# Optimization experiments

Measured on AMD Instinct MI355X. Metric: run time of the kernel, lower is better.

The kernel has to match this reference:

```python
import jax, jax.numpy as jnp
import numpy as np


def _swiglu(h):
    a, b = jnp.split(h, 2, axis=-1)
    return jax.nn.silu(a) * b


def setup_inputs() -> dict:
    key = jax.random.key(0)
    ks = jax.random.split(key, 12)
    B, T, D = 4, 2048, 1024
    HD = 4096          # dense FFN hidden (swiglu -> fc1 out 2*HD)
    S, K = 1024, 4     # ssm d_state, d_conv
    E, HE = 8, 512     # n_experts, expert hidden (swiglu)
    s = 0.02
    w = lambda k_, shape: jax.random.normal(k_, shape, jnp.float32) * s
    return dict(
        x=jax.random.normal(ks[0], (B, T, D), jnp.float32),
        rW=w(ks[1], (3, D)), rb=jnp.zeros((3,), jnp.float32),
        d1W=w(ks[2], (2 * HD, D)), d1b=jnp.zeros((2 * HD,), jnp.float32),
        d2W=w(ks[3], (D, HD)), d2b=jnp.zeros((D,), jnp.float32),
        sW_in=w(ks[4], (S, D)), sb_in=jnp.zeros((S,), jnp.float32),
        sW_conv=w(ks[5], (S, S, K)), sb_conv=jnp.zeros((S,), jnp.float32),
        sW_out=w(ks[6], (D, S)), sb_out=jnp.zeros((D,), jnp.float32),
        mW=w(ks[7], (E, D)), mb=jnp.zeros((E,), jnp.float32),
        eW1=w(ks[8], (E, 2 * HE, D)), eb1=jnp.zeros((E, 2 * HE), jnp.float32),
        eW2=w(ks[9], (E, D, HE)), eb2=jnp.zeros((E, D), jnp.float32),
        k=2,
    )


def reference(x, rW, rb, d1W, d1b, d2W, d2b,
              sW_in, sb_in, sW_conv, sb_conv, sW_out, sb_out,
              mW, mb, eW1, eb1, eW2, eb2, k):
    # ---- branch router (token-level softmax, temperature=1) ----
    bw = jax.nn.softmax(x @ rW.T + rb, axis=-1)              # [B,T,3]

    # ---- branch 0: dense swiglu FFN ----
    dense = _swiglu(x @ d1W.T + d1b) @ d2W.T + d2b           # [B,T,D]

    # ---- branch 1: SSM layer (causal conv, groups=1, gate=1) ----
    h = (x @ sW_in.T + sb_in).transpose(0, 2, 1)             # [B,S,T]
    Kc = sW_conv.shape[-1]
    conv = jax.lax.conv_general_dilated(
        h, sW_conv, window_strides=(1,), padding=[(Kc - 1, 0)],
        dimension_numbers=('NCH', 'OIH', 'NCH'))
    seq = (conv + sb_conv[None, :, None]).transpose(0, 2, 1)  # [B,T,S]
    ssm = seq @ sW_out.T + sb_out                             # [B,T,D]

    # ---- branch 2: MoE (top-k softmax router, dense-dispatch reference) ----
    E = mW.shape[0]
    logits = x @ mW.T + mb                                    # [B,T,E]
    vals, idx = jax.lax.top_k(logits, k)                      # [B,T,k]
    wk = jax.nn.softmax(vals, axis=-1)
    combine = jnp.sum(jax.nn.one_hot(idx, E, dtype=x.dtype) * wk[..., None], axis=-2)  # [B,T,E]
    h1 = _swiglu(jnp.einsum('btd,efd->btef', x, eW1) + eb1)   # [B,T,E,HE]
    eout = jnp.einsum('bteh,edh->bted', h1, eW2) + eb2        # [B,T,E,D]
    moe = jnp.einsum('bted,bte->btd', eout, combine)          # [B,T,D]

    return bw[..., 0:1] * dense + bw[..., 1:2] * ssm + bw[..., 2:3] * moe
```

## Files before the change

kernel.cpp:

```cpp
#include <hip/hip_runtime.h>
#include <hip/hip_bf16.h>
#include <cstdint>

typedef __bf16 bf16_t;
typedef __bf16 bf16x8 __attribute__((ext_vector_type(8)));
typedef float f32x4 __attribute__((ext_vector_type(4)));

#define DEV_INLINE __device__ __forceinline__

#define NTOK 8192
#define DDIM 1024
#define HDIM 4096
#define SDIM 1024
#define NEXP 8
#define HEXP 512
#define TSEQ 2048
#define MAXTILES 136
#define MAXROWS (MAXTILES * 128)

#define VMCNT(n) asm volatile("s_waitcnt vmcnt(" #n ")" ::: "memory")
#define BARF() asm volatile("s_barrier" ::: "memory")

__global__ __launch_bounds__(256) void k_f32_to_bf16(const float* __restrict__ src,
                                                     bf16_t* __restrict__ dst, int n8) {
  int i = blockIdx.x * 256 + threadIdx.x;
  if (i >= n8) return;
  const float4* s = (const float4*)src + (size_t)i * 2;
  float4 v0 = s[0], v1 = s[1];
  bf16x8 o;
  o[0] = (bf16_t)v0.x; o[1] = (bf16_t)v0.y; o[2] = (bf16_t)v0.z; o[3] = (bf16_t)v0.w;
  o[4] = (bf16_t)v1.x; o[5] = (bf16_t)v1.y; o[6] = (bf16_t)v1.z; o[7] = (bf16_t)v1.w;
  *((bf16x8*)dst + i) = o;
}

__global__ __launch_bounds__(256) void k_convw(const float* __restrict__ src,
                                               bf16_t* __restrict__ dst) {
  int i = blockIdx.x * 256 + threadIdx.x;
  size_t flat = (size_t)i * 8;
  int s = (int)(flat >> 12);
  int col = (int)(flat & 4095);
  int k = col >> 10;
  int si0 = col & 1023;
  const float* sp = src + (size_t)s * 4096 + k;
  bf16x8 o;
#pragma unroll
  for (int j = 0; j < 8; ++j) o[j] = (bf16_t)sp[(size_t)(si0 + j) * 4];
  *(bf16x8*)(dst + flat) = o;
}

__global__ __launch_bounds__(256) void k_zero(int* cnt, int* fill, int* idx,
                                              bf16_t* zpad) {
  int i = blockIdx.x * 256 + threadIdx.x;
  if (i < NEXP) { cnt[i] = 0; fill[i] = 0; }
  if (i < 128) zpad[i] = (bf16_t)0.f;
  if (i < MAXROWS) idx[i] = 0;
}

__global__ __launch_bounds__(1024) void k_count(const int* __restrict__ top2e,
                                                int* __restrict__ cnt) {
  __shared__ int hist[NEXP];
  const int tid = threadIdx.x;
  if (tid < NEXP) hist[tid] = 0;
  __syncthreads();
  int c[NEXP];
#pragma unroll
  for (int e = 0; e < NEXP; ++e) c[e] = 0;
#pragma unroll
  for (int j = 0; j < 2 * NTOK / 1024; ++j) {
    int v = top2e[j * 1024 + tid];
#pragma unroll
    for (int e = 0; e < NEXP; ++e) c[e] += (v == e) ? 1 : 0;
  }
#pragma unroll
  for (int e = 0; e < NEXP; ++e)
    for (int off = 32; off; off >>= 1) c[e] += __shfl_xor(c[e], off);
  if ((tid & 63) == 0) {
#pragma unroll
    for (int e = 0; e < NEXP; ++e) atomicAdd(&hist[e], c[e]);
  }
  __syncthreads();
  if (tid < NEXP) cnt[tid] = hist[tid];
}

__global__ void k_scan(const int* __restrict__ cnt, int* __restrict__ base,
                       int* __restrict__ ntiles, int* __restrict__ tile_e,
                       int* __restrict__ tile_row) {
  if (threadIdx.x == 0 && blockIdx.x == 0) {
    int b = 0, tt = 0;
    for (int e = 0; e < NEXP; ++e) {
      base[e] = b;
      int nt = (cnt[e] + 127) >> 7;
      for (int j = 0; j < nt; ++j) { tile_e[tt] = e; tile_row[tt] = b + j * 128; ++tt; }
      b += nt * 128;
    }
    *ntiles = tt;
  }
}

__global__ __launch_bounds__(256) void k_scatter(const int* __restrict__ top2e,
                                                 const float* __restrict__ top2w,
                                                 const int* __restrict__ base,
                                                 int* __restrict__ fill,
                                                 int* __restrict__ idx,
                                                 int* __restrict__ slotmap) {
  __shared__ int lcnt[NEXP];
  __shared__ int lbase[NEXP];
  const int tid = threadIdx.x;
  const int t = blockIdx.x * 256 + tid;
  if (tid < NEXP) lcnt[tid] = 0;
  __syncthreads();
  const int e0 = top2e[t * 2 + 0], e1 = top2e[t * 2 + 1];
  const int s0 = atomicAdd(&lcnt[e0], 1);
  const int s1 = atomicAdd(&lcnt[e1], 1);
  __syncthreads();
  if (tid < NEXP) lbase[tid] = atomicAdd(&fill[tid], lcnt[tid]);
  __syncthreads();
  const int p0 = base[e0] + lbase[e0] + s0;
  const int p1 = base[e1] + lbase[e1] + s1;
  idx[p0] = t; idx[p1] = t;
  slotmap[t * 2 + 0] = p0;
  slotmap[t * 2 + 1] = p1;
}

__global__ __launch_bounds__(256) void k_router(const float* __restrict__ x,
                                                const float* __restrict__ rW,
                                                const float* __restrict__ rb,
                                                const float* __restrict__ mW,
                                                const float* __restrict__ mb,
                                                float* __restrict__ bw3,
                                                int* __restrict__ top2e,
                                                float* __restrict__ top2w) {
  int wave = threadIdx.x >> 6, lane = threadIdx.x & 63;
  int t = blockIdx.x * 4 + wave;
  const float* xr = x + (size_t)t * DDIM;
  float xv[16];
#pragma unroll
  for (int i = 0; i < 16; i += 4) *(float4*)&xv[i] = *(const float4*)&xr[lane * 16 + i];
  float acc[11];
#pragma unroll
  for (int j = 0; j < 11; ++j) {
    const float* w = (j < 3) ? (rW + j * DDIM) : (mW + (j - 3) * DDIM);
    float s = 0.f;
#pragma unroll
    for (int i = 0; i < 16; i += 4) {
      float4 wv = *(const float4*)&w[lane * 16 + i];
      s += xv[i] * wv.x + xv[i + 1] * wv.y + xv[i + 2] * wv.z + xv[i + 3] * wv.w;
    }
    acc[j] = s;
  }
#pragma unroll
  for (int j = 0; j < 11; ++j)
    for (int off = 32; off; off >>= 1) acc[j] += __shfl_xor(acc[j], off);
  if (lane == 0) {
    float l0 = acc[0] + rb[0], l1 = acc[1] + rb[1], l2 = acc[2] + rb[2];
    float mx = fmaxf(l0, fmaxf(l1, l2));
    float e0 = expf(l0 - mx), e1 = expf(l1 - mx), e2 = expf(l2 - mx);
    float inv = 1.f / (e0 + e1 + e2);
    float w2 = e2 * inv;
    bw3[t * 3 + 0] = e0 * inv; bw3[t * 3 + 1] = e1 * inv; bw3[t * 3 + 2] = w2;
    float lg[8];
#pragma unroll
    for (int e = 0; e < 8; ++e) lg[e] = acc[3 + e] + mb[e];
    int i0 = 0;
#pragma unroll
    for (int e = 1; e < 8; ++e) if (lg[e] > lg[i0]) i0 = e;
    int i1 = -1;
#pragma unroll
    for (int e = 0; e < 8; ++e) {
      if (e == i0) continue;
      if (i1 < 0 || lg[e] > lg[i1]) i1 = e;
    }
    float ee = expf(lg[i1] - lg[i0]);
    float w0 = 1.f / (1.f + ee), w1 = ee / (1.f + ee);
    top2e[t * 2 + 0] = i0; top2e[t * 2 + 1] = i1;
    top2w[t * 2 + 0] = w2 * w0; top2w[t * 2 + 1] = w2 * w1;
  }
}

__global__ __launch_bounds__(256) void k_combine(const bf16_t* __restrict__ eo,
                                                 const int* __restrict__ slotmap,
                                                 const float* __restrict__ top2w,
                                                 float* __restrict__ out) {
  int wave = threadIdx.x >> 6, lane = threadIdx.x & 63;
  int t = blockIdx.x * 4 + wave;
  const int s0 = slotmap[t * 2 + 0], s1 = slotmap[t * 2 + 1];
  const float g0 = top2w[t * 2 + 0], g1 = top2w[t * 2 + 1];
  const bf16x8* r0 = (const bf16x8*)(eo + (size_t)s0 * DDIM);
  const bf16x8* r1 = (const bf16x8*)(eo + (size_t)s1 * DDIM);
  float* orow = out + (size_t)t * DDIM;
#pragma unroll
  for (int i = 0; i < 2; ++i) {
    const int d = lane + i * 64;
    bf16x8 a = r0[d], b = r1[d];
    float vo[8];
    *(float4*)&vo[0] = *(const float4*)&orow[d * 8];
    *(float4*)&vo[4] = *(const float4*)&orow[d * 8 + 4];
#pragma unroll
    for (int j = 0; j < 8; ++j) vo[j] += g0 * (float)a[j] + g1 * (float)b[j];
    *(float4*)&orow[d * 8] = *(float4*)&vo[0];
    *(float4*)&orow[d * 8 + 4] = *(float4*)&vo[4];
  }
}

DEV_INLINE void gload16(const bf16_t* g, bf16_t* l) {
  __builtin_amdgcn_global_load_lds((const __attribute__((address_space(1))) void*)g,
                                   (__attribute__((address_space(3))) void*)l, 16, 0, 0);
}

DEV_INLINE void blockmap(int K, int& bx, int& by) {
  const int nbx = gridDim.x, nby = gridDim.y;
  int id = blockIdx.x + nbx * blockIdx.y;
  const int nwg = nbx * nby;
  if ((nwg & 7) == 0) id = (id & 7) * (nwg >> 3) + (id >> 3);
  if ((nbx & 3) == 0 && (nby & 7) == 0 && K <= 2048) {
    const int nsx = nbx >> 2;
    const int sx = id & 3, r = id >> 2;
    const int sy = r & 7, st = r >> 3;
    bx = (st % nsx) * 4 + sx;
    by = (st / nsx) * 8 + sy;
  } else {
    bx = id % nbx;
    by = id / nbx;
  }
}

constexpr int EPI_BF16 = 0;
constexpr int EPI_OUT_W = 1;
constexpr int EPI_OUT_A = 2;
constexpr int EPI_SWIG = 4;

template <int EPI>
__global__ __launch_bounds__(256) void k_gemm(
    const bf16_t* __restrict__ A, const bf16_t* __restrict__ B,
    bf16_t* __restrict__ Cb, float* __restrict__ Cf,
    const float* __restrict__ bias, const float* __restrict__ scale, int sstride,
    const bf16_t* __restrict__ aux, int ldaux,
    int N, int K) {
  constexpr int BUF = 16384;
  __shared__ __align__(16) char lds[2 * BUF];

  const int tid = threadIdx.x;
  const int lane = tid & 63;
  const int wave = tid >> 6;
  const int lr = lane & 15;
  const int hi = lane >> 4;

  int bx, by;
  blockmap(K, bx, by);

  const int bm = by * 128;
  const int bn = bx * 128;
  const int wm = (wave >> 1) * 64;
  const int wn = (wave & 1) * 64;

  const int srow = tid >> 2;
  const int scol = 8 * ((tid & 3) ^ ((tid >> 3) & 3));
  const bf16_t* Asrc = A + (size_t)(bm + srow) * K + scol;
  const bf16_t* Bsrc = B + (size_t)(bn + srow) * K + scol;
  const size_t r64K = (size_t)64 * K;
  const int NT = K >> 5;

  f32x4 acc[4][4];
#pragma unroll
  for (int a = 0; a < 4; ++a)
#pragma unroll
    for (int b = 0; b < 4; ++b)
#pragma unroll
      for (int j = 0; j < 4; ++j) acc[a][b][j] = 0.f;

  auto stage = [&](int t) {
    char* l = lds + (t & 1) * BUF + tid * 16;
    const bf16_t* ga = Asrc + (size_t)t * 32;
    const bf16_t* gb = Bsrc + (size_t)t * 32;
    gload16(ga, (bf16_t*)l);
    gload16(ga + r64K, (bf16_t*)(l + 4096));
    gload16(gb, (bf16_t*)(l + 8192));
    gload16(gb + r64K, (bf16_t*)(l + 12288));
  };
  auto rdA = [&](int buf, int row) -> bf16x8 {
    int off = buf + (row << 6) + ((hi ^ ((row >> 1) & 3)) << 4);
    return *(const bf16x8*)(lds + off);
  };
  auto rdB = [&](int buf, int row) -> bf16x8 {
    int off = buf + 8192 + (row << 6) + ((hi ^ ((row >> 1) & 3)) << 4);
    return *(const bf16x8*)(lds + off);
  };

  stage(0);

  for (int t = 0; t < NT; ++t) {
    VMCNT(0);
    BARF();
    const int buf = (t & 1) * BUF;
    bf16x8 bfr[4], afr[4];
#pragma unroll
    for (int ni = 0; ni < 4; ++ni) bfr[ni] = rdB(buf, wn + ni * 16 + lr);
#pragma unroll
    for (int i = 0; i < 4; ++i) afr[i] = rdA(buf, wm + i * 16 + lr);
    if (t + 1 < NT) stage(t + 1);
    __builtin_amdgcn_s_setprio(1);
#pragma unroll
    for (int i = 0; i < 4; ++i)
#pragma unroll
      for (int ni = 0; ni < 4; ++ni)
        acc[i][ni] = __builtin_amdgcn_mfma_f32_16x16x32_bf16(afr[i], bfr[ni], acc[i][ni], 0, 0, 0);
    __builtin_amdgcn_s_setprio(0);
  }

  float bv[4];
#pragma unroll
  for (int ni = 0; ni < 4; ++ni) bv[ni] = bias[bn + wn + ni * 16 + lr];
#pragma unroll
  for (int mi = 0; mi < 4; ++mi) {
#pragma unroll
    for (int j = 0; j < 4; ++j) {
      const int rowg = bm + wm + mi * 16 + hi * 4 + j;
      float sc = 0.f;
      if constexpr (EPI == EPI_OUT_W || EPI == EPI_OUT_A)
        sc = scale[(size_t)rowg * sstride];
#pragma unroll
      for (int ni = 0; ni < 4; ++ni) {
        const int colg = bn + wn + ni * 16 + lr;
        float v = acc[mi][ni][j] + bv[ni];
        if constexpr (EPI == EPI_BF16) {
          Cb[(size_t)rowg * N + colg] = (bf16_t)v;
        } else if constexpr (EPI == EPI_OUT_W) {
          Cf[(size_t)rowg * N + colg] = sc * v;
        } else if constexpr (EPI == EPI_OUT_A) {
          Cf[(size_t)rowg * N + colg] += sc * v;
        } else {
          float bb = (float)aux[(size_t)rowg * ldaux + colg];
          float s = v / (1.f + __expf(-v));
          Cb[(size_t)rowg * N + colg] = (bf16_t)(s * bb);
        }
      }
    }
  }
}

__global__ __launch_bounds__(256) void k_gemm_conv(
    const bf16_t* __restrict__ h, const bf16_t* __restrict__ Bw,
    bf16_t* __restrict__ Cb, const float* __restrict__ bias,
    const bf16_t* __restrict__ zpad) {
  constexpr int N = SDIM;
  constexpr int K = SDIM * 4;
  constexpr int BUF = 16384;
  __shared__ __align__(16) char lds[2 * BUF];

  const int tid = threadIdx.x;
  const int lane = tid & 63;
  const int wave = tid >> 6;
  const int lr = lane & 15;
  const int hi = lane >> 4;

  int bx, by;
  blockmap(K, bx, by);

  const int bm = by * 128;
  const int bn = bx * 128;
  const int wm = (wave >> 1) * 64;
  const int wn = (wave & 1) * 64;

  const int srow = tid >> 2;
  const int scol = 8 * ((tid & 3) ^ ((tid >> 3) & 3));
  const int row0 = bm + srow;
  const int tt0 = row0 & (TSEQ - 1);
  const bf16_t* Bsrc = Bw + (size_t)(bn + srow) * K + scol;
  const size_t r64K = (size_t)64 * K;
  const int NT = K >> 5;

  f32x4 acc[4][4];
#pragma unroll
  for (int a = 0; a < 4; ++a)
#pragma unroll
    for (int b = 0; b < 4; ++b)
#pragma unroll
      for (int j = 0; j < 4; ++j) acc[a][b][j] = 0.f;

  auto stage = [&](int t) {
    char* l = lds + (t & 1) * BUF + tid * 16;
    const int k = t >> 5;
    const int si = (t & 31) * 32 + scol;
    const bf16_t* ga0 = (tt0 + k >= 3)
        ? h + (size_t)(row0 + k - 3) * SDIM + si : zpad;
    const bf16_t* ga1 = h + (size_t)(row0 + 64 + k - 3) * SDIM + si;
    gload16(ga0, (bf16_t*)l);
    gload16(ga1, (bf16_t*)(l + 4096));
    const bf16_t* gb = Bsrc + (size_t)t * 32;
    gload16(gb, (bf16_t*)(l + 8192));
    gload16(gb + r64K, (bf16_t*)(l + 12288));
  };
  auto rdA = [&](int buf, int row) -> bf16x8 {
    int off = buf + (row << 6) + ((hi ^ ((row >> 1) & 3)) << 4);
    return *(const bf16x8*)(lds + off);
  };
  auto rdB = [&](int buf, int row) -> bf16x8 {
    int off = buf + 8192 + (row << 6) + ((hi ^ ((row >> 1) & 3)) << 4);
    return *(const bf16x8*)(lds + off);
  };

  stage(0);

  for (int t = 0; t < NT; ++t) {
    VMCNT(0);
    BARF();
    const int buf = (t & 1) * BUF;
    bf16x8 bfr[4], afr[4];
#pragma unroll
    for (int ni = 0; ni < 4; ++ni) bfr[ni] = rdB(buf, wn + ni * 16 + lr);
#pragma unroll
    for (int i = 0; i < 4; ++i) afr[i] = rdA(buf, wm + i * 16 + lr);
    if (t + 1 < NT) stage(t + 1);
    __builtin_amdgcn_s_setprio(1);
#pragma unroll
    for (int i = 0; i < 4; ++i)
#pragma unroll
      for (int ni = 0; ni < 4; ++ni)
        acc[i][ni] = __builtin_amdgcn_mfma_f32_16x16x32_bf16(afr[i], bfr[ni], acc[i][ni], 0, 0, 0);
    __builtin_amdgcn_s_setprio(0);
  }

  float bv[4];
#pragma unroll
  for (int ni = 0; ni < 4; ++ni) bv[ni] = bias[bn + wn + ni * 16 + lr];
#pragma unroll
  for (int mi = 0; mi < 4; ++mi) {
#pragma unroll
    for (int j = 0; j < 4; ++j) {
      const int rowg = bm + wm + mi * 16 + hi * 4 + j;
#pragma unroll
      for (int ni = 0; ni < 4; ++ni) {
        const int colg = bn + wn + ni * 16 + lr;
        Cb[(size_t)rowg * N + colg] = (bf16_t)(acc[mi][ni][j] + bv[ni]);
      }
    }
  }
}

template <int EPI, bool GA>
__global__ __launch_bounds__(256) void k_moe_gemm(
    const bf16_t* __restrict__ A, const bf16_t* __restrict__ Bw, size_t zB, int boff,
    bf16_t* __restrict__ Cb,
    const float* __restrict__ bias, int bstride,
    const bf16_t* __restrict__ aux,
    const int* __restrict__ ntiles_p, const int* __restrict__ tile_e,
    const int* __restrict__ tile_row, const int* __restrict__ idx,
    int N, int K) {
  constexpr int BUF = 16384;
  __shared__ __align__(16) char lds[2 * BUF];

  const int tid = threadIdx.x;
  const int lane = tid & 63;
  const int wave = tid >> 6;
  const int lr = lane & 15;
  const int hi = lane >> 4;

  const int nbx = gridDim.x, nby = gridDim.y;
  int id = blockIdx.x + nbx * blockIdx.y;
  const int nwg = nbx * nby;
  if ((nwg & 7) == 0) id = (id & 7) * (nwg >> 3) + (id >> 3);
  const int bx = id % nbx;
  const int by = id / nbx;

  const int ntiles = *ntiles_p;
  if (bx >= ntiles) return;
  const int e = tile_e[bx];
  const int bm = tile_row[bx];
  const int bn = by * 128;
  const int wm = (wave >> 1) * 64;
  const int wn = (wave & 1) * 64;

  const int srow = tid >> 2;
  const int scol = 8 * ((tid & 3) ^ ((tid >> 3) & 3));
  const int atok0 = GA ? idx[bm + srow] : (bm + srow);
  const int atok1 = GA ? idx[bm + srow + 64] : (bm + srow + 64);
  const bf16_t* Asrc0 = A + (size_t)atok0 * K + scol;
  const bf16_t* Asrc1 = A + (size_t)atok1 * K + scol;
  const bf16_t* Bsrc = Bw + (size_t)e * zB + (size_t)(boff + bn + srow) * K + scol;
  const size_t r64K = (size_t)64 * K;
  const int NT = K >> 5;

  f32x4 acc[4][4];
#pragma unroll
  for (int a = 0; a < 4; ++a)
#pragma unroll
    for (int b = 0; b < 4; ++b)
#pragma unroll
      for (int j = 0; j < 4; ++j) acc[a][b][j] = 0.f;

  auto stage = [&](int t) {
    char* l = lds + (t & 1) * BUF + tid * 16;
    gload16(Asrc0 + (size_t)t * 32, (bf16_t*)l);
    gload16(Asrc1 + (size_t)t * 32, (bf16_t*)(l + 4096));
    gload16(Bsrc + (size_t)t * 32, (bf16_t*)(l + 8192));
    gload16(Bsrc + (size_t)t * 32 + r64K, (bf16_t*)(l + 12288));
  };
  auto rdA = [&](int buf, int row) -> bf16x8 {
    int off = buf + (row << 6) + ((hi ^ ((row >> 1) & 3)) << 4);
    return *(const bf16x8*)(lds + off);
  };
  auto rdB = [&](int buf, int row) -> bf16x8 {
    int off = buf + 8192 + (row << 6) + ((hi ^ ((row >> 1) & 3)) << 4);
    return *(const bf16x8*)(lds + off);
  };

  stage(0);

  for (int t = 0; t < NT; ++t) {
    VMCNT(0);
    BARF();
    const int buf = (t & 1) * BUF;
    bf16x8 bfr[4], afr[4];
#pragma unroll
    for (int ni = 0; ni < 4; ++ni) bfr[ni] = rdB(buf, wn + ni * 16 + lr);
#pragma unroll
    for (int i = 0; i < 4; ++i) afr[i] = rdA(buf, wm + i * 16 + lr);
    if (t + 1 < NT) stage(t + 1);
    __builtin_amdgcn_s_setprio(1);
#pragma unroll
    for (int i = 0; i < 4; ++i)
#pragma unroll
      for (int ni = 0; ni < 4; ++ni)
        acc[i][ni] = __builtin_amdgcn_mfma_f32_16x16x32_bf16(afr[i], bfr[ni], acc[i][ni], 0, 0, 0);
    __builtin_amdgcn_s_setprio(0);
  }

  const float* bp = bias + (size_t)e * bstride + boff;
  float bv[4];
#pragma unroll
  for (int ni = 0; ni < 4; ++ni) bv[ni] = bp[bn + wn + ni * 16 + lr];
#pragma unroll
  for (int mi = 0; mi < 4; ++mi) {
#pragma unroll
    for (int j = 0; j < 4; ++j) {
      const int slot = bm + wm + mi * 16 + hi * 4 + j;
#pragma unroll
      for (int ni = 0; ni < 4; ++ni) {
        const int colg = bn + wn + ni * 16 + lr;
        float v = acc[mi][ni][j] + bv[ni];
        if constexpr (EPI == EPI_BF16) {
          Cb[(size_t)slot * N + colg] = (bf16_t)v;
        } else {
          float bb = (float)aux[(size_t)slot * N + colg];
          float s = v / (1.f + __expf(-v));
          Cb[(size_t)slot * N + colg] = (bf16_t)(s * bb);
        }
      }
    }
  }
}

extern "C" void kernel_launch(void* const* d_in, const int* in_sizes, int n_in,
                              void* d_out, int out_size, void* d_ws, size_t ws_size,
                              hipStream_t stream) {
  (void)in_sizes; (void)n_in; (void)out_size; (void)ws_size;
  const float* x    = (const float*)d_in[0];
  const float* rW   = (const float*)d_in[1];
  const float* rb   = (const float*)d_in[2];
  const float* d1W  = (const float*)d_in[3];
  const float* d1b  = (const float*)d_in[4];
  const float* d2W  = (const float*)d_in[5];
  const float* d2b  = (const float*)d_in[6];
  const float* sWin = (const float*)d_in[7];
  const float* sbin = (const float*)d_in[8];
  const float* sWc  = (const float*)d_in[9];
  const float* sbc  = (const float*)d_in[10];
  const float* sWo  = (const float*)d_in[11];
  const float* sbo  = (const float*)d_in[12];
  const float* mW   = (const float*)d_in[13];
  const float* mb   = (const float*)d_in[14];
  const float* eW1  = (const float*)d_in[15];
  const float* eb1  = (const float*)d_in[16];
  const float* eW2  = (const float*)d_in[17];
  const float* eb2  = (const float*)d_in[18];
  float* out = (float*)d_out;

  char* ws = (char*)d_ws;
  size_t off = 0;
  auto alloc = [&](size_t bytes) -> void* {
    void* p = ws + off;
    off += (bytes + 255) & ~(size_t)255;
    return p;
  };
  bf16_t* xb    = (bf16_t*)alloc((size_t)NTOK * DDIM * 2);
  bf16_t* wd1   = (bf16_t*)alloc((size_t)2 * HDIM * DDIM * 2);
  bf16_t* wd2   = (bf16_t*)alloc((size_t)DDIM * HDIM * 2);
  bf16_t* wsin  = (bf16_t*)alloc((size_t)SDIM * DDIM * 2);
  bf16_t* wconv = (bf16_t*)alloc((size_t)SDIM * SDIM * 4 * 2);
  bf16_t* wsout = (bf16_t*)alloc((size_t)DDIM * SDIM * 2);
  bf16_t* we1   = (bf16_t*)alloc((size_t)NEXP * 2 * HEXP * DDIM * 2);
  bf16_t* we2   = (bf16_t*)alloc((size_t)NEXP * DDIM * HEXP * 2);
  bf16_t* Cc    = (bf16_t*)alloc((size_t)NTOK * HDIM * 2);
  bf16_t* Dd    = (bf16_t*)alloc((size_t)NTOK * HDIM * 2);
  bf16_t* th    = (bf16_t*)alloc((size_t)NTOK * SDIM * 2);
  bf16_t* tsq   = (bf16_t*)alloc((size_t)NTOK * SDIM * 2);
  float*  bw3   = (float*)alloc((size_t)NTOK * 3 * 4);
  int*    top2e = (int*)alloc((size_t)NTOK * 2 * 4);
  float*  top2w = (float*)alloc((size_t)NTOK * 2 * 4);
  int*    slotm = (int*)alloc((size_t)NTOK * 2 * 4);
  int*    cnt   = (int*)alloc(NEXP * 4);
  int*    fill  = (int*)alloc(NEXP * 4);
  int*    basep = (int*)alloc((NEXP + 1) * 4);
  int*    ntl   = (int*)alloc(4);
  int*    t_e   = (int*)alloc(MAXTILES * 4);
  int*    t_row = (int*)alloc(MAXTILES * 4);
  int*    idx   = (int*)alloc(MAXROWS * 4);
  bf16_t* zpad  = (bf16_t*)alloc(256);
  bf16_t* eo    = Dd;

  k_f32_to_bf16<<<4096, 256, 0, stream>>>(x, xb, NTOK * DDIM / 8);
  k_f32_to_bf16<<<4096, 256, 0, stream>>>(d1W, wd1, 2 * HDIM * DDIM / 8);
  k_f32_to_bf16<<<2048, 256, 0, stream>>>(d2W, wd2, DDIM * HDIM / 8);
  k_f32_to_bf16<<<512, 256, 0, stream>>>(sWin, wsin, SDIM * DDIM / 8);
  k_convw<<<2048, 256, 0, stream>>>(sWc, wconv);
  k_f32_to_bf16<<<512, 256, 0, stream>>>(sWo, wsout, DDIM * SDIM / 8);
  k_f32_to_bf16<<<4096, 256, 0, stream>>>(eW1, we1, NEXP * 2 * HEXP * DDIM / 8);
  k_f32_to_bf16<<<2048, 256, 0, stream>>>(eW2, we2, NEXP * DDIM * HEXP / 8);
  k_zero<<<(MAXROWS + 255) / 256, 256, 0, stream>>>(cnt, fill, idx, zpad);
  k_router<<<2048, 256, 0, stream>>>(x, rW, rb, mW, mb, bw3, top2e, top2w);
  k_count<<<1, 1024, 0, stream>>>(top2e, cnt);
  k_scan<<<1, 64, 0, stream>>>(cnt, basep, ntl, t_e, t_row);
  k_scatter<<<NTOK / 256, 256, 0, stream>>>(top2e, top2w, basep, fill, idx, slotm);

  k_gemm<EPI_BF16><<<dim3(32, 64), 256, 0, stream>>>(
      xb, wd1 + (size_t)HDIM * DDIM, Dd, nullptr, d1b + HDIM, nullptr, 0, nullptr, 0,
      HDIM, DDIM);
  k_gemm<EPI_SWIG><<<dim3(32, 64), 256, 0, stream>>>(
      xb, wd1, Cc, nullptr, d1b, nullptr, 0, Dd, HDIM, HDIM, DDIM);
  k_gemm<EPI_OUT_W><<<dim3(8, 64), 256, 0, stream>>>(
      Cc, wd2, nullptr, out, d2b, bw3, 3, nullptr, 0, DDIM, HDIM);

  k_moe_gemm<EPI_BF16, true><<<dim3(MAXTILES, 4), 256, 0, stream>>>(
      xb, we1, (size_t)2 * HEXP * DDIM, HEXP, Dd, eb1, 2 * HEXP, nullptr,
      ntl, t_e, t_row, idx, HEXP, DDIM);
  k_moe_gemm<EPI_SWIG, true><<<dim3(MAXTILES, 4), 256, 0, stream>>>(
      xb, we1, (size_t)2 * HEXP * DDIM, 0, Cc, eb1, 2 * HEXP, Dd,
      ntl, t_e, t_row, idx, HEXP, DDIM);
  k_moe_gemm<EPI_BF16, false><<<dim3(MAXTILES, 8), 256, 0, stream>>>(
      Cc, we2, (size_t)DDIM * HEXP, 0, eo, eb2, DDIM, nullptr,
      ntl, t_e, t_row, idx, DDIM, HEXP);
  k_combine<<<NTOK / 4, 256, 0, stream>>>(eo, slotm, top2w, out);

  k_gemm<EPI_BF16><<<dim3(8, 64), 256, 0, stream>>>(
      xb, wsin, th, nullptr, sbin, nullptr, 0, nullptr, 0, SDIM, DDIM);
  k_gemm_conv<<<dim3(8, 64), 256, 0, stream>>>(th, wconv, tsq, sbc, zpad);
  k_gemm<EPI_OUT_A><<<dim3(8, 64), 256, 0, stream>>>(
      tsq, wsout, nullptr, out, sbo, bw3 + 1, 3, nullptr, 0, DDIM, SDIM);
}
```

Before: 669.9 us.

## Fuse SwiGLU gate and up GEMMs into one dual-accumulator kernel

The dense FC1 and the MoE expert FC1 each used to run as two GEMMs: one wrote the up half to a bf16 buffer, and the second read it back in a SwiGLU epilogue. They are now single kernels that stage A once, load both weight halves into a larger LDS buffer, keep two accumulator sets, and apply silu(a)*b directly in the epilogue. This removes a full intermediate write/read and one read of the activations. The cost is double the accumulator registers, which can lower occupancy or cause spills. The grouped block-swizzle mapping in blockmap is also dropped in favour of a plain row-major mapping, which may change L2 reuse.

After: 691.9 us. 3.3% more time.

```diff
diff --git a/kernel.cpp b/kernel.cpp
--- a/kernel.cpp
+++ b/kernel.cpp
@@ -207,34 +207,24 @@
                                    (__attribute__((address_space(3))) void*)l, 16, 0, 0);
 }
 
-DEV_INLINE void blockmap(int K, int& bx, int& by) {
+DEV_INLINE void blockmap(int& bx, int& by) {
   const int nbx = gridDim.x, nby = gridDim.y;
   int id = blockIdx.x + nbx * blockIdx.y;
   const int nwg = nbx * nby;
   if ((nwg & 7) == 0) id = (id & 7) * (nwg >> 3) + (id >> 3);
-  if ((nbx & 3) == 0 && (nby & 7) == 0 && K <= 2048) {
-    const int nsx = nbx >> 2;
-    const int sx = id & 3, r = id >> 2;
-    const int sy = r & 7, st = r >> 3;
-    bx = (st % nsx) * 4 + sx;
-    by = (st / nsx) * 8 + sy;
-  } else {
-    bx = id % nbx;
-    by = id / nbx;
-  }
+  bx = id % nbx;
+  by = id / nbx;
 }
 
 constexpr int EPI_BF16 = 0;
 constexpr int EPI_OUT_W = 1;
 constexpr int EPI_OUT_A = 2;
-constexpr int EPI_SWIG = 4;
 
 template <int EPI>
 __global__ __launch_bounds__(256) void k_gemm(
     const bf16_t* __restrict__ A, const bf16_t* __restrict__ B,
     bf16_t* __restrict__ Cb, float* __restrict__ Cf,
     const float* __restrict__ bias, const float* __restrict__ scale, int sstride,
-    const bf16_t* __restrict__ aux, int ldaux,
     int N, int K) {
   constexpr int BUF = 16384;
   __shared__ __align__(16) char lds[2 * BUF];
@@ -246,7 +236,7 @@
   const int hi = lane >> 4;
 
   int bx, by;
-  blockmap(K, bx, by);
+  blockmap(bx, by);
 
   const int bm = by * 128;
   const int bn = bx * 128;
@@ -326,13 +316,112 @@
           Cb[(size_t)rowg * N + colg] = (bf16_t)v;
         } else if constexpr (EPI == EPI_OUT_W) {
           Cf[(size_t)rowg * N + colg] = sc * v;
-        } else if constexpr (EPI == EPI_OUT_A) {
+        } else {
           Cf[(size_t)rowg * N + colg] += sc * v;
-        } else {
-          float bb = (float)aux[(size_t)rowg * ldaux + colg];
-          float s = v / (1.f + __expf(-v));
-          Cb[(size_t)rowg * N + colg] = (bf16_t)(s * bb);
         }
+      }
+    }
+  }
+}
+
+__global__ __launch_bounds__(256) void k_gemm_fc1(
+    const bf16_t* __restrict__ A, const bf16_t* __restrict__ Ba,
+    const bf16_t* __restrict__ Bb, bf16_t* __restrict__ C,
+    const float* __restrict__ bias_a, const float* __restrict__ bias_b,
+    int N, int K) {
+  constexpr int BUF = 24576;
+  __shared__ __align__(16) char lds[2 * BUF];
+
+  const int tid = threadIdx.x;
+  const int lane = tid & 63;
+  const int wave = tid >> 6;
+  const int lr = lane & 15;
+  const int hi = lane >> 4;
+
+  int bx, by;
+  blockmap(bx, by);
+
+  const int bm = by * 128;
+  const int bn = bx * 128;
+  const int wm = (wave >> 1) * 64;
+  const int wn = (wave & 1) * 64;
+
+  const int srow = tid >> 2;
+  const int scol = 8 * ((tid & 3) ^ ((tid >> 3) & 3));
+  const bf16_t* Asrc = A + (size_t)(bm + srow) * K + scol;
+  const bf16_t* Basrc = Ba + (size_t)(bn + srow) * K + scol;
+  const bf16_t* Bbsrc = Bb + (size_t)(bn + srow) * K + scol;
+  const size_t r64K = (size_t)64 * K;
+  const int NT = K >> 5;
+
+  f32x4 aca[4][4], acb[4][4];
+#pragma unroll
+  for (int a = 0; a < 4; ++a)
+#pragma unroll
+    for (int b = 0; b < 4; ++b)
+#pragma unroll
+      for (int j = 0; j < 4; ++j) { aca[a][b][j] = 0.f; acb[a][b][j] = 0.f; }
+
+  auto stage = [&](int t) {
+    char* l = lds + (t & 1) * BUF + tid * 16;
+    const bf16_t* ga = Asrc + (size_t)t * 32;
+    const bf16_t* gba = Basrc + (size_t)t * 32;
+    const bf16_t* gbb = Bbsrc + (size_t)t * 32;
+    gload16(ga, (bf16_t*)l);
+    gload16(ga + r64K, (bf16_t*)(l + 4096));
+    gload16(gba, (bf16_t*)(l + 8192));
+    gload16(gba + r64K, (bf16_t*)(l + 12288));
+    gload16(gbb, (bf16_t*)(l + 16384));
+    gload16(gbb + r64K, (bf16_t*)(l + 20480));
+  };
+  auto rd = [&](int base, int row) -> bf16x8 {
+    int off = base + (row << 6) + ((hi ^ ((row >> 1) & 3)) << 4);
+    return *(const bf16x8*)(lds + off);
+  };
+
+  stage(0);
+
+  for (int t = 0; t < NT; ++t) {
+    VMCNT(0);
+    BARF();
+    const int buf = (t & 1) * BUF;
+    bf16x8 afr[4], bfa[4], bfb[4];
+#pragma unroll
+    for (int i = 0; i < 4; ++i) afr[i] = rd(buf, wm + i * 16 + lr);
+#pragma unroll
+    for (int ni = 0; ni < 4; ++ni) bfa[ni] = rd(buf + 8192, wn + ni * 16 + lr);
+#pragma unroll
+    for (int ni = 0; ni < 4; ++ni) bfb[ni] = rd(buf + 16384, wn + ni * 16 + lr);
+    if (t + 1 < NT) stage(t + 1);
+    __builtin_amdgcn_s_setprio(1);
+#pragma unroll
+    for (int i = 0; i < 4; ++i)
+#pragma unroll
+      for (int ni = 0; ni < 4; ++ni) {
+        aca[i][ni] = __builtin_amdgcn_mfma_f32_16x16x32_bf16(afr[i], bfa[ni], aca[i][ni], 0, 0, 0);
+        acb[i][ni] = __builtin_amdgcn_mfma_f32_16x16x32_bf16(afr[i], bfb[ni], acb[i][ni], 0, 0, 0);
+      }
+    __builtin_amdgcn_s_setprio(0);
+  }
+
+  float bva[4], bvb[4];
+#pragma unroll
+  for (int ni = 0; ni < 4; ++ni) {
+    bva[ni] = bias_a[bn + wn + ni * 16 + lr];
+    bvb[ni] = bias_b[bn + wn + ni * 16 + lr];
+  }
+#pragma unroll
+  for (int mi = 0; mi < 4; ++mi) {
+#pragma unroll
+    for (int j = 0; j < 4; ++j) {
+      const int rowg = bm + wm + mi * 16 + hi * 4 + j;
+#pragma unroll
+      for (int ni = 0; ni < 4; ++ni) {
+        const int colg = bn + wn + ni * 16 + lr;
+        float va = aca[mi][ni][j] + bva[ni];
+        float vb = acb[mi][ni][j] + bvb[ni];
+        float s = va / (1.f + __expf(-va));
+        C[(size_t)rowg * N + colg] = (bf16_t)(s * vb);
       }
     }
   }
@@ -354,7 +443,7 @@
   const int hi = lane >> 4;
 
   int bx, by;
-  blockmap(K, bx, by);
+  blockmap(bx, by);
 
   const int bm = by * 128;
   const int bn = bx * 128;
@@ -437,16 +526,13 @@
   }
 }
 
-template <int EPI, bool GA>
-__global__ __launch_bounds__(256) void k_moe_gemm(
-    const bf16_t* __restrict__ A, const bf16_t* __restrict__ Bw, size_t zB, int boff,
-    bf16_t* __restrict__ Cb,
-    const float* __restrict__ bias, int bstride,
-    const bf16_t* __restrict__ aux,
+__global__ __launch_bounds__(256) void k_moe_fc1(
+    const bf16_t* __restrict__ A, const bf16_t* __restrict__ Bw, size_t zB,
+    bf16_t* __restrict__ C, const float* __restrict__ bias, int bstride,
     const int* __restrict__ ntiles_p, const int* __restrict__ tile_e,
     const int* __restrict__ tile_row, const int* __restrict__ idx,
     int N, int K) {
-  constexpr int BUF = 16384;
+  constexpr int BUF = 24576;
   __shared__ __align__(16) char lds[2 * BUF];
 
   const int tid = threadIdx.x;
@@ -472,26 +558,136 @@
 
   const int srow = tid >> 2;
   const int scol = 8 * ((tid & 3) ^ ((tid >> 3) & 3));
-  const int atok0 = GA ? idx[bm + srow] : (bm + srow);
-  const int atok1 = GA ? idx[bm + srow + 64] : (bm + srow + 64);
+  const int atok0 = idx[bm + srow];
+  const int atok1 = idx[bm + srow + 64];
   const bf16_t* Asrc0 = A + (size_t)atok0 * K + scol;
   const bf16_t* Asrc1 = A + (size_t)atok1 * K + scol;
-  const bf16_t* Bsrc = Bw + (size_t)e * zB + (size_t)(boff + bn + srow) * K + scol;
+  const bf16_t* Basrc = Bw + (size_t)e * zB + (size_t)(bn + srow) * K + scol;
+  const bf16_t* Bbsrc = Basrc + (size_t)HEXP * K;
   const size_t r64K = (size_t)64 * K;
   const int NT = K >> 5;
 
-  f32x4 acc[4][4];
+  f32x4 aca[4][4], acb[4][4];
 #pragma unroll
   for (int a = 0; a < 4; ++a)
 #pragma unroll
     for (int b = 0; b < 4; ++b)
 #pragma unroll
-      for (int j = 0; j < 4; ++j) acc[a][b][j] = 0.f;
+      for (int j = 0; j < 4; ++j) { aca[a][b][j] = 0.f; acb[a][b][j] = 0.f; }
 
   auto stage = [&](int t) {
     char* l = lds + (t & 1) * BUF + tid * 16;
     gload16(Asrc0 + (size_t)t * 32, (bf16_t*)l);
     gload16(Asrc1 + (size_t)t * 32, (bf16_t*)(l + 4096));
+    gload16(Basrc + (size_t)t * 32, (bf16_t*)(l + 8192));
+    gload16(Basrc + (size_t)t * 32 + r64K, (bf16_t*)(l + 12288));
+    gload16(Bbsrc + (size_t)t * 32, (bf16_t*)(l + 16384));
+    gload16(Bbsrc + (size_t)t * 32 + r64K, (bf16_t*)(l + 20480));
+  };
+  auto rd = [&](int base, int row) -> bf16x8 {
+    int off = base + (row << 6) + ((hi ^ ((row >> 1) & 3)) << 4);
+    return *(const bf16x8*)(lds + off);
+  };
+
+  stage(0);
+
+  for (int t = 0; t < NT; ++t) {
+    VMCNT(0);
+    BARF();
+    const int buf = (t & 1) * BUF;
+    bf16x8 afr[4], bfa[4], bfb[4];
+#pragma unroll
+    for (int i = 0; i < 4; ++i) afr[i] = rd(buf, wm + i * 16 + lr);
+#pragma unroll
+    for (int ni = 0; ni < 4; ++ni) bfa[ni] = rd(buf + 8192, wn + ni * 16 + lr);
+#pragma unroll
+    for (int ni = 0; ni < 4; ++ni) bfb[ni] = rd(buf + 16384, wn + ni * 16 + lr);
+    if (t + 1 < NT) stage(t + 1);
+    __builtin_amdgcn_s_setprio(1);
+#pragma unroll
+    for (int i = 0; i < 4; ++i)
+#pragma unroll
+      for (int ni = 0; ni < 4; ++ni) {
+        aca[i][ni] = __builtin_amdgcn_mfma_f32_16x16x32_bf16(afr[i], bfa[ni], aca[i][ni], 0, 0, 0);
+        acb[i][ni] = __builtin_amdgcn_mfma_f32_16x16x32_bf16(afr[i], bfb[ni], acb[i][ni], 0, 0, 0);
+      }
+    __builtin_amdgcn_s_setprio(0);
+  }
+
+  const float* bpa = bias + (size_t)e * bstride;
+  const float* bpb = bpa + HEXP;
+  float bva[4], bvb[4];
+#pragma unroll
+  for (int ni = 0; ni < 4; ++ni) {
+    bva[ni] = bpa[bn + wn + ni * 16 + lr];
+    bvb[ni] = bpb[bn + wn + ni * 16 + lr];
+  }
+#pragma unroll
+  for (int mi = 0; mi < 4; ++mi) {
+#pragma unroll
+    for (int j = 0; j < 4; ++j) {
+      const int slot = bm + wm + mi * 16 + hi * 4 + j;
+#pragma unroll
+      for (int ni = 0; ni < 4; ++ni) {
+        const int colg = bn + wn + ni * 16 + lr;
+        float va = aca[mi][ni][j] + bva[ni];
+        float vb = acb[mi][ni][j] + bvb[ni];
+        float s = va / (1.f + __expf(-va));
+        C[(size_t)slot * N + colg] = (bf16_t)(s * vb);
+      }
+    }
+  }
+}
+
+__global__ __launch_bounds__(256) void k_moe_fc2(
+    const bf16_t* __restrict__ A, const bf16_t* __restrict__ Bw, size_t zB,
+    bf16_t* __restrict__ Cb, const float* __restrict__ bias, int bstride,
+    const int* __restrict__ ntiles_p, const int* __restrict__ tile_e,
+    const int* __restrict__ tile_row,
+    int N, int K) {
+  constexpr int BUF = 16384;
+  __shared__ __align__(16) char lds[2 * BUF];
+
+  const int tid = threadIdx.x;
+  const int lane = tid & 63;
+  const int wave = tid >> 6;
+  const int lr = lane & 15;
+  const int hi = lane >> 4;
+
+  const int nbx = gridDim.x, nby = gridDim.y;
+  int id = blockIdx.x + nbx * blockIdx.y;
+  const int nwg = nbx * nby;
+  if ((nwg & 7) == 0) id = (id & 7) * (nwg >> 3) + (id >> 3);
+  const int bx = id % nbx;
+  const int by = id / nbx;
+
+  const int ntiles = *ntiles_p;
+  if (bx >= ntiles) return;
+  const int e = tile_e[bx];
+  const int bm = tile_row[bx];
+  const int bn = by * 128;
+  const int wm = (wave >> 1) * 64;
+  const int wn = (wave & 1) * 64;
+
+  const int srow = tid >> 2;
+  const int scol = 8 * ((tid & 3) ^ ((tid >> 3) & 3));
+  const bf16_t* Asrc = A + (size_t)(bm + srow) * K + scol;
+  const bf16_t* Bsrc = Bw + (size_t)e * zB + (size_t)(bn + srow) * K + scol;
+  const size_t r64K = (size_t)64 * K;
+  const int NT = K >> 5;
+
+  f32x4 acc[4][4];
+#pragma unroll
+  for (int a = 0; a < 4; ++a)
+#pragma unroll
+    for (int b = 0; b < 4; ++b)
+#pragma unroll
+      for (int j = 0; j < 4; ++j) acc[a][b][j] = 0.f;
+
+  auto stage = [&](int t) {
+    char* l = lds + (t & 1) * BUF + tid * 16;
+    gload16(Asrc + (size_t)t * 32, (bf16_t*)l);
+    gload16(Asrc + (size_t)t * 32 + r64K, (bf16_t*)(l + 4096));
     gload16(Bsrc + (size_t)t * 32, (bf16_t*)(l + 8192));
     gload16(Bsrc + (size_t)t * 32 + r64K, (bf16_t*)(l + 12288));
   };
@@ -525,7 +721,7 @@
     __builtin_amdgcn_s_setprio(0);
   }
 
-  const float* bp = bias + (size_t)e * bstride + boff;
+  const float* bp = bias + (size_t)e * bstride;
   float bv[4];
 #pragma unroll
   for (int ni = 0; ni < 4; ++ni) bv[ni] = bp[bn + wn + ni * 16 + lr];
@@ -537,14 +733,7 @@
 #pragma unroll
       for (int ni = 0; ni < 4; ++ni) {
         const int colg = bn + wn + ni * 16 + lr;
-        float v = acc[mi][ni][j] + bv[ni];
-        if constexpr (EPI == EPI_BF16) {
-          Cb[(size_t)slot * N + colg] = (bf16_t)v;
-        } else {
-          float bb = (float)aux[(size_t)slot * N + colg];
-          float s = v / (1.f + __expf(-v));
-          Cb[(size_t)slot * N + colg] = (bf16_t)(s * bb);
-        }
+        Cb[(size_t)slot * N + colg] = (bf16_t)(acc[mi][ni][j] + bv[ni]);
       }
     }
   }
@@ -622,28 +811,22 @@
   k_scan<<<1, 64, 0, stream>>>(cnt, basep, ntl, t_e, t_row);
   k_scatter<<<NTOK / 256, 256, 0, stream>>>(top2e, top2w, basep, fill, idx, slotm);
 
-  k_gemm<EPI_BF16><<<dim3(32, 64), 256, 0, stream>>>(
-      xb, wd1 + (size_t)HDIM * DDIM, Dd, nullptr, d1b + HDIM, nullptr, 0, nullptr, 0,
-      HDIM, DDIM);
-  k_gemm<EPI_SWIG><<<dim3(32, 64), 256, 0, stream>>>(
-      xb, wd1, Cc, nullptr, d1b, nullptr, 0, Dd, HDIM, HDIM, DDIM);
+  k_gemm_fc1<<<dim3(32, 64), 256, 0, stream>>>(
+      xb, wd1, wd1 + (size_t)HDIM * DDIM, Cc, d1b, d1b + HDIM, HDIM, DDIM);
   k_gemm<EPI_OUT_W><<<dim3(8, 64), 256, 0, stream>>>(
-      Cc, wd2, nullptr, out, d2b, bw3, 3, nullptr, 0, DDIM, HDIM);
-
-  k_moe_gemm<EPI_BF16, true><<<dim3(MAXTILES, 4), 256, 0, stream>>>(
-      xb, we1, (size_t)2 * HEXP * DDIM, HEXP, Dd, eb1, 2 * HEXP, nullptr,
+      Cc, wd2, nullptr, out, d2b, bw3, 3, DDIM, HDIM);
+
+  k_moe_fc1<<<dim3(MAXTILES, 4), 256, 0, stream>>>(
+      xb, we1, (size_t)2 * HEXP * DDIM, Cc, eb1, 2 * HEXP,
       ntl, t_e, t_row, idx, HEXP, DDIM);
-  k_moe_gemm<EPI_SWIG, true><<<dim3(MAXTILES, 4), 256, 0, stream>>>(
-      xb, we1, (size_t)2 * HEXP * DDIM, 0, Cc, eb1, 2 * HEXP, Dd,
-      ntl, t_e, t_row, idx, HEXP, DDIM);
-  k_moe_gemm<EPI_BF16, false><<<dim3(MAXTILES, 8), 256, 0, stream>>>(
-      Cc, we2, (size_t)DDIM * HEXP, 0, eo, eb2, DDIM, nullptr,
-      ntl, t_e, t_row, idx, DDIM, HEXP);
+  k_moe_fc2<<<dim3(MAXTILES, 8), 256, 0, stream>>>(
+      Cc, we2, (size_t)DDIM * HEXP, eo, eb2, DDIM,
+      ntl, t_e, t_row, DDIM, HEXP);
   k_combine<<<NTOK / 4, 256, 0, stream>>>(eo, slotm, top2w, out);
 
   k_gemm<EPI_BF16><<<dim3(8, 64), 256, 0, stream>>>(
-      xb, wsin, th, nullptr, sbin, nullptr, 0, nullptr, 0, SDIM, DDIM);
+      xb, wsin, th, nullptr, sbin, nullptr, 0, SDIM, DDIM);
   k_gemm_conv<<<dim3(8, 64), 256, 0, stream>>>(th, wconv, tsq, sbc, zpad);
   k_gemm<EPI_OUT_A><<<dim3(8, 64), 256, 0, stream>>>(
-      tsq, wsout, nullptr, out, sbo, bw3 + 1, 3, nullptr, 0, DDIM, SDIM);
-}
+      tsq, wsout, nullptr, out, sbo, bw3 + 1, 3, DDIM, SDIM);
+}
```
